# Performance work log

Measured on AMD Instinct MI355X. Metric: run time of the kernel, lower is better.

Reference implementation:

```python
import jax, jax.numpy as jnp
import numpy as np

N, E = 100000, 1600000
D_IN, D_HID, D_OUT, P_HID = 256, 128, 128, 512
BN_EPS = 1e-5


def setup_inputs():
    key = jax.random.key(0)
    ks = jax.random.split(key, 16)
    rn = lambda k, sh, s: jax.random.normal(k, sh, jnp.float32) * s
    inp = {
        "x1": rn(ks[0], (N, D_IN), 1.0),
        "x2": rn(ks[1], (N, D_IN), 1.0),
        "edge_index_v1": jax.random.randint(ks[2], (2, E), 0, N, dtype=jnp.int32),
        "edge_index_v2": jax.random.randint(ks[3], (2, E), 0, N, dtype=jnp.int32),
    }
    # student (s_) and teacher (t_) encoder params: GCN weight/bias, BN gamma/beta, PReLU a
    for i, p in enumerate(("s", "t")):
        kk = jax.random.split(ks[4 + i], 4)
        inp[p + "_W1"] = rn(kk[0], (D_IN, D_HID), (2.0 / (D_IN + D_HID)) ** 0.5)
        inp[p + "_b1"] = jnp.zeros((D_HID,), jnp.float32)
        inp[p + "_g1"] = jnp.ones((D_HID,), jnp.float32)
        inp[p + "_be1"] = jnp.zeros((D_HID,), jnp.float32)
        inp[p + "_a1"] = jnp.float32(0.25)
        inp[p + "_W2"] = rn(kk[1], (D_HID, D_OUT), (2.0 / (D_HID + D_OUT)) ** 0.5)
        inp[p + "_b2"] = jnp.zeros((D_OUT,), jnp.float32)
        inp[p + "_g2"] = jnp.ones((D_OUT,), jnp.float32)
        inp[p + "_be2"] = jnp.zeros((D_OUT,), jnp.float32)
        inp[p + "_a2"] = jnp.float32(0.25)
    kk = jax.random.split(ks[6], 2)
    inp["p_W1"] = rn(kk[0], (D_OUT, P_HID), (2.0 / (D_OUT + P_HID)) ** 0.5)
    inp["p_b1"] = jnp.full((P_HID,), 0.01, jnp.float32)
    inp["p_a"] = jnp.float32(0.25)
    inp["p_W2"] = rn(kk[1], (P_HID, D_OUT), (2.0 / (P_HID + D_OUT)) ** 0.5)
    inp["p_b2"] = jnp.full((D_OUT,), 0.01, jnp.float32)
    return inp


def _add_self_loops(edge_index, n):
    loops = jnp.arange(n, dtype=edge_index.dtype)
    return (jnp.concatenate([edge_index[0], loops]),
            jnp.concatenate([edge_index[1], loops]))


def _gcn(x, src, dst, W, b):
    # torch_geometric GCNConv: symmetric deg^-1/2 norm, transform then scatter-add, bias after
    n = x.shape[0]
    ew = jnp.ones(src.shape, x.dtype)
    deg = jax.ops.segment_sum(ew, dst, num_segments=n)
    dinv = jnp.where(deg > 0, jax.lax.rsqrt(deg), 0.0)
    norm = (dinv[src] * dinv[dst])[:, None]  # [E+N, 1]
    h = x @ W  # [N, d_out]
    out = jax.ops.segment_sum(h[src] * norm, dst, num_segments=n)
    return out + b


def _bn(x, g, b):
    mu = x.mean(0)
    var = ((x - mu) ** 2).mean(0)  # biased var, training-mode batch stats
    return (x - mu) * jax.lax.rsqrt(var + BN_EPS) * g + b


def _prelu(x, a):
    return jnp.where(x >= 0, x, a * x)


def _encoder(x, src, dst, p):
    W1, b1, g1, be1, a1, W2, b2, g2, be2, a2 = p
    h = _prelu(_bn(_gcn(x, src, dst, W1, b1), g1, be1), a1)
    return _prelu(_bn(_gcn(h, src, dst, W2, b2), g2, be2), a2)


def _normalize(x):
    return x / jnp.maximum(jnp.linalg.norm(x, axis=-1, keepdims=True), 1e-12)


def reference(x1, x2, edge_index_v1, edge_index_v2,
              s_W1, s_b1, s_g1, s_be1, s_a1, s_W2, s_b2, s_g2, s_be2, s_a2,
              t_W1, t_b1, t_g1, t_be1, t_a1, t_W2, t_b2, t_g2, t_be2, t_a2,
              p_W1, p_b1, p_a, p_W2, p_b2):
    n = x1.shape[0]
    src1, dst1 = _add_self_loops(edge_index_v1, n)
    src2, dst2 = _add_self_loops(edge_index_v2, n)
    sp = (s_W1, s_b1, s_g1, s_be1, s_a1, s_W2, s_b2, s_g2, s_be2, s_a2)
    tp = (t_W1, t_b1, t_g1, t_be1, t_a1, t_W2, t_b2, t_g2, t_be2, t_a2)

    v1_student = _encoder(x1, src1, dst1, sp)
    v2_student = _encoder(x2, src2, dst2, sp)

    def _pred(h):
        return _prelu(h @ p_W1 + p_b1, p_a) @ p_W2 + p_b2

    v1_pred = _pred(v1_student)
    v2_pred = _pred(v2_student)

    v1_teacher = jax.lax.stop_gradient(_encoder(x1, src1, dst1, tp))
    v2_teacher = jax.lax.stop_gradient(_encoder(x2, src2, dst2, tp))

    loss1 = 2.0 - 2.0 * (_normalize(v1_pred) * _normalize(v2_teacher)).sum(-1)
    loss2 = 2.0 - 2.0 * (_normalize(v2_pred) * _normalize(v1_teacher)).sum(-1)
    return (v1_student, v2_student, (loss1 + loss2).mean())
```

## Files before the change

kernel.cpp:

```cpp
#include <hip/hip_runtime.h>

#define NN 100000
#define EE 1600000
#define ENN (EE + NN)
#define DIN 256
#define DH 128
#define PH 512

static constexpr float BN_EPS_C = 1e-5f;

typedef __bf16 bf16_t;
typedef bf16_t bf16x8 __attribute__((ext_vector_type(8)));
typedef bf16_t bf16x4 __attribute__((ext_vector_type(4)));
typedef float floatx4 __attribute__((ext_vector_type(4)));


__global__ void init_deg_k(int* __restrict__ deg1, int* __restrict__ deg2) {
    int i = blockIdx.x * 256 + threadIdx.x;
    if (i < NN) { deg1[i] = 1; deg2[i] = 1; }
}

__global__ void count_deg_k(const int* __restrict__ dst, int* __restrict__ deg) {
    int e = blockIdx.x * 256 + threadIdx.x;
    if (e < EE) atomicAdd(&deg[dst[e]], 1);
}

__global__ void dinv_k(const int* __restrict__ deg, float* __restrict__ dinv) {
    int i = blockIdx.x * 256 + threadIdx.x;
    if (i < NN) dinv[i] = rsqrtf((float)deg[i]);
}

__global__ void scan1_k(const int* __restrict__ deg, int* __restrict__ bsum) {
    __shared__ int sh[256];
    int t = threadIdx.x;
    int base = blockIdx.x * 1024 + t * 4;
    int s = 0;
#pragma unroll
    for (int i = 0; i < 4; i++) { int idx = base + i; if (idx < NN) s += deg[idx]; }
    sh[t] = s; __syncthreads();
    for (int off = 128; off > 0; off >>= 1) { if (t < off) sh[t] += sh[t + off]; __syncthreads(); }
    if (t == 0) bsum[blockIdx.x] = sh[0];
}

__global__ void scan2_k(int* __restrict__ bsum, int nb) {
    __shared__ int sh[128];
    int t = threadIdx.x;
    int my = (t < nb) ? bsum[t] : 0;
    sh[t] = my; __syncthreads();
    for (int off = 1; off < 128; off <<= 1) {
        int v = (t >= off) ? sh[t - off] : 0;
        __syncthreads(); sh[t] += v; __syncthreads();
    }
    if (t < nb) bsum[t] = sh[t] - my;
}

__global__ void scan3_k(const int* __restrict__ deg, const int* __restrict__ bsum,
                        int* __restrict__ rowoff) {
    __shared__ int sh[256];
    int t = threadIdx.x;
    int base = blockIdx.x * 1024 + t * 4;
    int v[4]; int s = 0;
#pragma unroll
    for (int i = 0; i < 4; i++) { int idx = base + i; v[i] = (idx < NN) ? deg[idx] : 0; s += v[i]; }
    int my = s;
    sh[t] = s; __syncthreads();
    for (int off = 1; off < 256; off <<= 1) {
        int x = (t >= off) ? sh[t - off] : 0;
        __syncthreads(); sh[t] += x; __syncthreads();
    }
    int run = sh[t] - my + bsum[blockIdx.x];
#pragma unroll
    for (int i = 0; i < 4; i++) { int idx = base + i; if (idx < NN) rowoff[idx] = run; run += v[i]; }
    if (blockIdx.x == 0 && t == 0) rowoff[NN] = ENN;
}

__global__ void csr_init_k(const int* __restrict__ rowoff, const float* __restrict__ dinv,
                           int* __restrict__ cursor, int2* __restrict__ csre) {
    int i = blockIdx.x * 256 + threadIdx.x;
    if (i < NN) {
        int p = rowoff[i];
        float d = dinv[i];
        csre[p] = make_int2(i, __float_as_int(d * d));
        cursor[i] = p + 1;
    }
}

__global__ void csr_place_k(const int* __restrict__ src, const int* __restrict__ dst,
                            const float* __restrict__ dinv, int* __restrict__ cursor,
                            int2* __restrict__ csre) {
    int e = blockIdx.x * 256 + threadIdx.x;
    if (e < EE) {
        int s = src[e], d = dst[e];
        int p = atomicAdd(&cursor[d], 1);
        csre[p] = make_int2(s, __float_as_int(dinv[s] * dinv[d]));
    }
}


__global__ __launch_bounds__(256) void gather256_k(
    const int* __restrict__ ro, const int2* __restrict__ csre,
    const bf16_t* __restrict__ h,
    const float* __restrict__ bs, const float* __restrict__ bt,
    float* __restrict__ out)
{
    int wv = threadIdx.x >> 6, lane = threadIdx.x & 63;
    int d = blockIdx.x * 4 + wv;
    if (d >= NN) return;
    int beg = ro[d], end = ro[d + 1];
    int half = lane >> 5;
    int l32 = lane & 31;
    int c8 = l32 * 8;
    const bf16_t* hp = h + c8;
    float acc[8] = {0.f, 0.f, 0.f, 0.f, 0.f, 0.f, 0.f, 0.f};

    for (int e = beg; e < end; e += 8) {
        int i0 = e + half;
        int i1 = i0 + 2, i2 = i0 + 4, i3 = i0 + 6;
        bool val0 = i0 < end, val1 = i1 < end, val2 = i2 < end, val3 = i3 < end;
        int j0 = val0 ? i0 : end - 1;
        int j1 = val1 ? i1 : end - 1;
        int j2 = val2 ? i2 : end - 1;
        int j3 = val3 ? i3 : end - 1;
        int2 w0 = csre[j0];
        int2 w1 = csre[j1];
        int2 w2 = csre[j2];
        int2 w3 = csre[j3];
        uint4 p0 = *(const uint4*)(hp + w0.x * 256);
        uint4 p1 = *(const uint4*)(hp + w1.x * 256);
        uint4 p2 = *(const uint4*)(hp + w2.x * 256);
        uint4 p3 = *(const uint4*)(hp + w3.x * 256);
        float f0 = val0 ? __int_as_float(w0.y) : 0.f;
        float f1 = val1 ? __int_as_float(w1.y) : 0.f;
        float f2 = val2 ? __int_as_float(w2.y) : 0.f;
        float f3 = val3 ? __int_as_float(w3.y) : 0.f;
#define GACC(P, F) \
        acc[0] += (F) * __uint_as_float((P).x << 16); \
        acc[1] += (F) * __uint_as_float((P).x & 0xffff0000u); \
        acc[2] += (F) * __uint_as_float((P).y << 16); \
        acc[3] += (F) * __uint_as_float((P).y & 0xffff0000u); \
        acc[4] += (F) * __uint_as_float((P).z << 16); \
        acc[5] += (F) * __uint_as_float((P).z & 0xffff0000u); \
        acc[6] += (F) * __uint_as_float((P).w << 16); \
        acc[7] += (F) * __uint_as_float((P).w & 0xffff0000u);
        GACC(p0, f0)
        GACC(p1, f1)
        GACC(p2, f2)
        GACC(p3, f3)
#undef GACC
    }

#pragma unroll
    for (int j = 0; j < 8; j++) acc[j] += __shfl_xor(acc[j], 32);

    int cB = c8 + half * 4;
    int o = half * 4;
    float b0 = (cB < 128) ? bs[cB]     : bt[cB - 128];
    float b1 = (cB < 128) ? bs[cB + 1] : bt[cB - 127];
    float b2 = (cB < 128) ? bs[cB + 2] : bt[cB - 126];
    float b3 = (cB < 128) ? bs[cB + 3] : bt[cB - 125];
    float4 r = make_float4(acc[o] + b0, acc[o + 1] + b1, acc[o + 2] + b2, acc[o + 3] + b3);
    *(float4*)&out[(size_t)d * 256 + cB] = r;
}


#define GSTAT 1024
#define SROWS ((NN + GSTAT - 1) / GSTAT)

__global__ __launch_bounds__(256) void bn_stats_cat_k(const float* __restrict__ x,
                                                      float* __restrict__ stats) {
    __shared__ float sh[2][4][256];
    int t = threadIdx.x;
    int wv = t >> 6, lane = t & 63;
    int c4 = lane * 4;
    int rend = (blockIdx.x + 1) * SROWS; if (rend > NN) rend = NN;
    float4 s = make_float4(0.f, 0.f, 0.f, 0.f);
    float4 q = make_float4(0.f, 0.f, 0.f, 0.f);
    for (int r = blockIdx.x * SROWS + wv; r < rend; r += 4) {
        float4 v = *(const float4*)&x[(size_t)r * 256 + c4];
        s.x += v.x; s.y += v.y; s.z += v.z; s.w += v.w;
        q.x += v.x * v.x; q.y += v.y * v.y; q.z += v.z * v.z; q.w += v.w * v.w;
    }
    *(float4*)&sh[0][wv][c4] = s;
    *(float4*)&sh[1][wv][c4] = q;
    __syncthreads();
    if (t < 128) {
        int which = t >> 6;
        int c = (t & 63) * 4;
        float4 a  = *(float4*)&sh[which][0][c];
        float4 b  = *(float4*)&sh[which][1][c];
        float4 cc = *(float4*)&sh[which][2][c];
        float4 d  = *(float4*)&sh[which][3][c];
        atomicAdd(&stats[which * 256 + c],     a.x + b.x + cc.x + d.x);
        atomicAdd(&stats[which * 256 + c + 1], a.y + b.y + cc.y + d.y);
        atomicAdd(&stats[which * 256 + c + 2], a.z + b.z + cc.z + d.z);
        atomicAdd(&stats[which * 256 + c + 3], a.w + b.w + cc.w + d.w);
    }
}

__global__ void bn_prelu_cat_k(const float* __restrict__ x, const float* __restrict__ stats,
                               const float* __restrict__ gs, const float* __restrict__ gt,
                               const float* __restrict__ bes, const float* __restrict__ bet,
                               const float* __restrict__ as_, const float* __restrict__ at_,
                               bf16_t* __restrict__ out) {
    size_t i4 = ((size_t)blockIdx.x * 256 + threadIdx.x) * 4;
    if (i4 < (size_t)NN * 256) {
        int c = (int)(i4 & 255);
        bool st = c < 128;
        int cb = st ? c : c - 128;
        const float* gp  = st ? gs  : gt;
        const float* bep = st ? bes : bet;
        float al = st ? as_[0] : at_[0];
        float4 v = *(const float4*)&x[i4];
        float vv[4] = {v.x, v.y, v.z, v.w};
        bf16x4 o;
#pragma unroll
        for (int j = 0; j < 4; j++) {
            float mu  = stats[c + j] * (1.0f / NN);
            float var = stats[256 + c + j] * (1.0f / NN) - mu * mu;
            float sc  = rsqrtf(var + BN_EPS_C) * gp[cb + j];
            float r   = (vv[j] - mu) * sc + bep[cb + j];
            r = r >= 0.f ? r : al * r;
            o[j] = (bf16_t)r;
        }
        *(bf16x4*)&out[i4] = o;
    }
}

__global__ void bn_prelu_out_k(const float* __restrict__ x, const float* __restrict__ stats,
                               const float* __restrict__ gs, const float* __restrict__ gt,
                               const float* __restrict__ bes, const float* __restrict__ bet,
                               const float* __restrict__ as_, const float* __restrict__ at_,
                               float* __restrict__ outs, bf16_t* __restrict__ outsb,
                               bf16_t* __restrict__ outt) {
    size_t i4 = ((size_t)blockIdx.x * 256 + threadIdx.x) * 4;
    if (i4 >= (size_t)NN * 256) return;
    int c = (int)(i4 & 255);
    size_t r = i4 >> 8;
    bool st = c < 128;
    int cb = st ? c : c - 128;
    const float* gp  = st ? gs  : gt;
    const float* bep = st ? bes : bet;
    float al = st ? as_[0] : at_[0];
    float4 v = *(const float4*)&x[i4];
    float vv[4] = {v.x, v.y, v.z, v.w};
    float res[4];
    bf16x4 o;
#pragma unroll
    for (int j = 0; j < 4; j++) {
        float mu  = stats[c + j] * (1.0f / NN);
        float var = stats[256 + c + j] * (1.0f / NN) - mu * mu;
        float sc  = rsqrtf(var + BN_EPS_C) * gp[cb + j];
        float rr  = (vv[j] - mu) * sc + bep[cb + j];
        rr = rr >= 0.f ? rr : al * rr;
        res[j] = rr;
        o[j] = (bf16_t)rr;
    }
    if (st) {
        *(float4*)&outs[r * 128 + cb] = make_float4(res[0], res[1], res[2], res[3]);
        *(bf16x4*)&outsb[r * 128 + cb] = o;
    } else {
        *(bf16x4*)&outt[r * 128 + cb] = o;
    }
}


__global__ void wt_k(const float* __restrict__ W, bf16_t* __restrict__ Wt, int K, int M) {
    int i = blockIdx.x * 256 + threadIdx.x;
    if (i < K * M) {
        int k = i / M, m = i - k * M;
        Wt[(size_t)m * K + k] = (bf16_t)W[i];
    }
}


#define LDT 40

template <int K, typename AT, typename OT, bool BIAS, bool PRELU>
__global__ __launch_bounds__(256) void mgemm_k(
    const AT* __restrict__ A, int lda, const bf16_t* __restrict__ Wt,
    OT* __restrict__ C, int ldc, int nrows, int aoffy,
    const float* __restrict__ bias, const float* __restrict__ prelu_a)
{
    __shared__ __align__(16) bf16_t sA[128 * LDT];
    __shared__ __align__(16) bf16_t sB[128 * LDT];
    const int tid = threadIdx.x;
    const int row0 = blockIdx.x * 128;
    const int col0 = blockIdx.y * 128;
    const int lane = tid & 63, quad = lane >> 4, l15 = lane & 15;
    const int wv = tid >> 6, wrow = wv >> 1, wcol = wv & 1;

    const int sr = tid >> 1;
    const int sh = (tid & 1) * 16;

    floatx4 acc[4][4] = {};

    const int arow = row0 + sr;
    const bool arow_ok = arow < nrows;
    const AT*     ag = A  + (size_t)arow * lda + sh + blockIdx.y * aoffy;
    const bf16_t* bg = Wt + (size_t)(col0 + sr) * K + sh;

    for (int k0 = 0; k0 < K; k0 += 32) {
        __syncthreads();
        if constexpr (sizeof(AT) == 4) {
            float4 f0, f1, f2, f3;
            if (arow_ok) {
                const float4* p4 = (const float4*)(ag + k0);
                f0 = p4[0]; f1 = p4[1]; f2 = p4[2]; f3 = p4[3];
            } else {
                f0 = f1 = f2 = f3 = make_float4(0.f, 0.f, 0.f, 0.f);
            }
            bf16x8 u0 = {(bf16_t)f0.x, (bf16_t)f0.y, (bf16_t)f0.z, (bf16_t)f0.w,
                         (bf16_t)f1.x, (bf16_t)f1.y, (bf16_t)f1.z, (bf16_t)f1.w};
            bf16x8 u1 = {(bf16_t)f2.x, (bf16_t)f2.y, (bf16_t)f2.z, (bf16_t)f2.w,
                         (bf16_t)f3.x, (bf16_t)f3.y, (bf16_t)f3.z, (bf16_t)f3.w};
            *(bf16x8*)&sA[sr * LDT + sh]     = u0;
            *(bf16x8*)&sA[sr * LDT + sh + 8] = u1;
        } else {
            int4 w0, w1;
            if (arow_ok) {
                const int4* p4 = (const int4*)(ag + k0);
                w0 = p4[0]; w1 = p4[1];
            } else {
                w0 = make_int4(0, 0, 0, 0); w1 = make_int4(0, 0, 0, 0);
            }
            *(int4*)&sA[sr * LDT + sh]     = w0;
            *(int4*)&sA[sr * LDT + sh + 8] = w1;
        }
        {
            const int4* wp = (const int4*)(bg + k0);
            int4 w0 = wp[0], w1 = wp[1];
            *(int4*)&sB[sr * LDT + sh]     = w0;
            *(int4*)&sB[sr * LDT + sh + 8] = w1;
        }
        __syncthreads();

        bf16x8 af[4], bf[4];
#pragma unroll
        for (int r = 0; r < 4; r++)
            af[r] = *(const bf16x8*)&sA[(wrow * 64 + r * 16 + l15) * LDT + quad * 8];
#pragma unroll
        for (int c = 0; c < 4; c++)
            bf[c] = *(const bf16x8*)&sB[(wcol * 64 + c * 16 + l15) * LDT + quad * 8];
#pragma unroll
        for (int r = 0; r < 4; r++)
#pragma unroll
            for (int c = 0; c < 4; c++)
                acc[r][c] = __builtin_amdgcn_mfma_f32_16x16x32_bf16(af[r], bf[c], acc[r][c], 0, 0, 0);
    }

    const float alpha = PRELU ? prelu_a[0] : 0.f;
#pragma unroll
    for (int r = 0; r < 4; r++) {
        const int rbase = wrow * 64 + r * 16 + quad * 4;
#pragma unroll
        for (int c = 0; c < 4; c++) {
            const int gcol = col0 + wcol * 64 + c * 16 + l15;
            const float bv = BIAS ? bias[gcol] : 0.f;
#pragma unroll
            for (int j = 0; j < 4; j++) {
                const int grow = row0 + rbase + j;
                if (grow < nrows) {
                    float v = acc[r][c][j] + bv;
                    if (PRELU) v = v >= 0.f ? v : alpha * v;
                    C[(size_t)grow * ldc + gcol] = (OT)v;
                }
            }
        }
    }
}


__global__ void loss_partial_k(const bf16_t* __restrict__ v1p, const bf16_t* __restrict__ v2t,
                               const bf16_t* __restrict__ v2p, const bf16_t* __restrict__ v1t,
                               float* __restrict__ partials) {
    __shared__ float shw[4];
    int t = threadIdx.x;
    int lane = t & 63, wv = t >> 6;
    float wsum = 0.f;
    for (int it = 0; it < 8; ++it) {
        int r = blockIdx.x * 32 + wv * 8 + it;
        if (r < NN) {
            const bf16_t* A = v1p + (size_t)r * DH;
            const bf16_t* B = v2t + (size_t)r * DH;
            const bf16_t* Cc = v2p + (size_t)r * DH;
            const bf16_t* D = v1t + (size_t)r * DH;
            float a0 = (float)A[lane], a1 = (float)A[lane + 64];
            float b0 = (float)B[lane], b1 = (float)B[lane + 64];
            float c0 = (float)Cc[lane], c1 = (float)Cc[lane + 64];
            float d0 = (float)D[lane], d1 = (float)D[lane + 64];
            float dot1 = a0 * b0 + a1 * b1;
            float na = a0 * a0 + a1 * a1, nb = b0 * b0 + b1 * b1;
            float dot2 = c0 * d0 + c1 * d1;
            float nc = c0 * c0 + c1 * c1, nd = d0 * d0 + d1 * d1;
            for (int off = 32; off > 0; off >>= 1) {
                dot1 += __shfl_down(dot1, off);
                na   += __shfl_down(na, off);
                nb   += __shfl_down(nb, off);
                dot2 += __shfl_down(dot2, off);
                nc   += __shfl_down(nc, off);
                nd   += __shfl_down(nd, off);
            }
            if (lane == 0) {
                float den1 = fmaxf(sqrtf(na), 1e-12f) * fmaxf(sqrtf(nb), 1e-12f);
                float den2 = fmaxf(sqrtf(nc), 1e-12f) * fmaxf(sqrtf(nd), 1e-12f);
                wsum += 4.f - 2.f * dot1 / den1 - 2.f * dot2 / den2;
            }
        }
    }
    if (lane == 0) shw[wv] = wsum;
    __syncthreads();
    if (t == 0) partials[blockIdx.x] = shw[0] + shw[1] + shw[2] + shw[3];
}

__global__ void loss_final_k(const float* __restrict__ partials, int n, float* __restrict__ out) {
    __shared__ float sh[256];
    int t = threadIdx.x;
    float s = 0.f;
    for (int i = t; i < n; i += 256) s += partials[i];
    sh[t] = s; __syncthreads();
    for (int off = 128; off > 0; off >>= 1) { if (t < off) sh[t] += sh[t + off]; __syncthreads(); }
    if (t == 0) out[0] = sh[0] / (float)NN;
}


extern "C" void kernel_launch(void* const* d_in, const int* in_sizes, int n_in,
                              void* d_out, int out_size, void* d_ws, size_t ws_size,
                              hipStream_t stream) {
    const float* x1 = (const float*)d_in[0];
    const float* x2 = (const float*)d_in[1];
    const int* ei1 = (const int*)d_in[2];
    const int* ei2 = (const int*)d_in[3];
    const float* sp[10]; for (int i = 0; i < 10; i++) sp[i] = (const float*)d_in[4 + i];
    const float* tp[10]; for (int i = 0; i < 10; i++) tp[i] = (const float*)d_in[14 + i];
    const float* pW1 = (const float*)d_in[24];
    const float* pb1 = (const float*)d_in[25];
    const float* pa  = (const float*)d_in[26];
    const float* pW2 = (const float*)d_in[27];
    const float* pb2 = (const float*)d_in[28];

    float* out = (float*)d_out;
    float* v1s = out;
    float* v2s = out + (size_t)NN * DH;
    float* lossp = out + (size_t)2 * NN * DH;

    char* p = (char*)d_ws;
    auto alloc = [&](size_t bytes) { char* r = p; p += (bytes + 255) & ~(size_t)255; return r; };
    int*   deg1   = (int*)alloc(NN * 4);
    int*   deg2   = (int*)alloc(NN * 4);
    float* dinv1  = (float*)alloc(NN * 4);
    float* dinv2  = (float*)alloc(NN * 4);
    int*   ro1    = (int*)alloc((NN + 1) * 4);
    int*   ro2    = (int*)alloc((NN + 1) * 4);
    int*   cursor = (int*)alloc(NN * 4);
    int*   bsum   = (int*)alloc(128 * 4);
    int2*  csre1  = (int2*)alloc((size_t)ENN * 8);
    int2*  csre2  = (int2*)alloc((size_t)ENN * 8);
    bf16_t* hcat  = (bf16_t*)alloc((size_t)NN * 256 * 2);
    bf16_t* h2    = (bf16_t*)alloc((size_t)NN * 256 * 2);
    float*  agg   = (float*)alloc((size_t)NN * 256 * 4);
    bf16_t* v1sb  = (bf16_t*)alloc((size_t)NN * DH * 2);
    bf16_t* v2sb  = (bf16_t*)alloc((size_t)NN * DH * 2);
    bf16_t* v1t   = (bf16_t*)alloc((size_t)NN * DH * 2);
    bf16_t* v2t   = (bf16_t*)alloc((size_t)NN * DH * 2);
    bf16_t* v1p   = (bf16_t*)alloc((size_t)NN * DH * 2);
    bf16_t* v2p   = (bf16_t*)alloc((size_t)NN * DH * 2);
    float* stats  = (float*)alloc(4 * 512 * 4);
    float* partials = (float*)alloc(4096 * 4);
    bf16_t* W1cat = (bf16_t*)alloc((size_t)2 * DIN * DH * 2);
    bf16_t* W2cat = (bf16_t*)alloc((size_t)2 * DH * DH * 2);
    bf16_t* pW1t = (bf16_t*)alloc((size_t)DH * PH * 2);
    bf16_t* pW2t = (bf16_t*)alloc((size_t)PH * DH * 2);

    const int GN256 = (NN + 255) / 256;
    const int GE256 = (EE + 255) / 256;
    const int NB_SCAN = (NN + 1023) / 1024;
    const int GMM = (NN + 127) / 128;
    const int GG = (NN + 3) / 4;
    const int GEL4 = (NN * 256 / 4 + 255) / 256;

    hipMemsetAsync(stats, 0, 4 * 512 * 4, stream);

    wt_k<<<(DIN * DH + 255) / 256, 256, 0, stream>>>(sp[0], W1cat, DIN, DH);
    wt_k<<<(DIN * DH + 255) / 256, 256, 0, stream>>>(tp[0], W1cat + (size_t)DH * DIN, DIN, DH);
    wt_k<<<(DH * DH + 255) / 256, 256, 0, stream>>>(sp[5], W2cat, DH, DH);
    wt_k<<<(DH * DH + 255) / 256, 256, 0, stream>>>(tp[5], W2cat + (size_t)DH * DH, DH, DH);
    wt_k<<<(DH * PH + 255) / 256, 256, 0, stream>>>(pW1, pW1t, DH, PH);
    wt_k<<<(PH * DH + 255) / 256, 256, 0, stream>>>(pW2, pW2t, PH, DH);

    init_deg_k<<<GN256, 256, 0, stream>>>(deg1, deg2);
    count_deg_k<<<GE256, 256, 0, stream>>>(ei1 + EE, deg1);
    count_deg_k<<<GE256, 256, 0, stream>>>(ei2 + EE, deg2);
    dinv_k<<<GN256, 256, 0, stream>>>(deg1, dinv1);
    dinv_k<<<GN256, 256, 0, stream>>>(deg2, dinv2);

    scan1_k<<<NB_SCAN, 256, 0, stream>>>(deg1, bsum);
    scan2_k<<<1, 128, 0, stream>>>(bsum, NB_SCAN);
    scan3_k<<<NB_SCAN, 256, 0, stream>>>(deg1, bsum, ro1);
    csr_init_k<<<GN256, 256, 0, stream>>>(ro1, dinv1, cursor, csre1);
    csr_place_k<<<GE256, 256, 0, stream>>>(ei1, ei1 + EE, dinv1, cursor, csre1);

    scan1_k<<<NB_SCAN, 256, 0, stream>>>(deg2, bsum);
    scan2_k<<<1, 128, 0, stream>>>(bsum, NB_SCAN);
    scan3_k<<<NB_SCAN, 256, 0, stream>>>(deg2, bsum, ro2);
    csr_init_k<<<GN256, 256, 0, stream>>>(ro2, dinv2, cursor, csre2);
    csr_place_k<<<GE256, 256, 0, stream>>>(ei2, ei2 + EE, dinv2, cursor, csre2);

    auto encoder = [&](const float* x, const int* ro, const int2* csre,
                       float* vs_out, bf16_t* vsb, bf16_t* vt, int set) {
        mgemm_k<DIN, float, bf16_t, false, false><<<dim3(GMM, 2), 256, 0, stream>>>(
            x, DIN, W1cat, hcat, 256, NN, 0, nullptr, nullptr);
        gather256_k<<<GG, 256, 0, stream>>>(ro, csre, hcat, sp[1], tp[1], agg);
        bn_stats_cat_k<<<GSTAT, 256, 0, stream>>>(agg, stats + set * 512);
        bn_prelu_cat_k<<<GEL4, 256, 0, stream>>>(agg, stats + set * 512,
            sp[2], tp[2], sp[3], tp[3], sp[4], tp[4], hcat);
        mgemm_k<DH, bf16_t, bf16_t, false, false><<<dim3(GMM, 2), 256, 0, stream>>>(
            hcat, 256, W2cat, h2, 256, NN, 128, nullptr, nullptr);
        gather256_k<<<GG, 256, 0, stream>>>(ro, csre, h2, sp[6], tp[6], agg);
        bn_stats_cat_k<<<GSTAT, 256, 0, stream>>>(agg, stats + (set + 1) * 512);
        bn_prelu_out_k<<<GEL4, 256, 0, stream>>>(agg, stats + (set + 1) * 512,
            sp[7], tp[7], sp[8], tp[8], sp[9], tp[9], vs_out, vsb, vt);
    };

    encoder(x1, ro1, csre1, v1s, v1sb, v1t, 0);
    encoder(x2, ro2, csre2, v2s, v2sb, v2t, 2);

    bf16_t* hid = (bf16_t*)agg;
    auto predictor = [&](const bf16_t* vin, bf16_t* vout) {
        mgemm_k<DH, bf16_t, bf16_t, true, true><<<dim3(GMM, PH / 128), 256, 0, stream>>>(
            vin, DH, pW1t, hid, PH, NN, 0, pb1, pa);
        mgemm_k<PH, bf16_t, bf16_t, true, false><<<dim3(GMM, 1), 256, 0, stream>>>(
            hid, PH, pW2t, vout, DH, NN, 0, pb2, nullptr);
    };
    predictor(v1sb, v1p);
    predictor(v2sb, v2p);

    const int GL = (NN + 31) / 32;
    loss_partial_k<<<GL, 256, 0, stream>>>(v1p, v2t, v2p, v1t, partials);
    loss_final_k<<<1, 256, 0, stream>>>(partials, GL, lossp);
}
```

Measured before the change: 2.041 ms.

## Fuse BN statistics into gather, BN-PReLU into GEMM load, batch predictor views

```diff
diff --git a/kernel.cpp b/kernel.cpp
--- a/kernel.cpp
+++ b/kernel.cpp
@@ -97,92 +97,82 @@
 }
 
 
+#define GGB 2048
+
 __global__ __launch_bounds__(256) void gather256_k(
     const int* __restrict__ ro, const int2* __restrict__ csre,
     const bf16_t* __restrict__ h,
     const float* __restrict__ bs, const float* __restrict__ bt,
-    float* __restrict__ out)
+    float* __restrict__ out, float* __restrict__ stats)
 {
     int wv = threadIdx.x >> 6, lane = threadIdx.x & 63;
-    int d = blockIdx.x * 4 + wv;
-    if (d >= NN) return;
-    int beg = ro[d], end = ro[d + 1];
     int half = lane >> 5;
     int l32 = lane & 31;
     int c8 = l32 * 8;
     const bf16_t* hp = h + c8;
-    float acc[8] = {0.f, 0.f, 0.f, 0.f, 0.f, 0.f, 0.f, 0.f};
-
-    for (int e = beg; e < end; e += 8) {
-        int i0 = e + half;
-        int i1 = i0 + 2, i2 = i0 + 4, i3 = i0 + 6;
-        bool val0 = i0 < end, val1 = i1 < end, val2 = i2 < end, val3 = i3 < end;
-        int j0 = val0 ? i0 : end - 1;
-        int j1 = val1 ? i1 : end - 1;
-        int j2 = val2 ? i2 : end - 1;
-        int j3 = val3 ? i3 : end - 1;
-        int2 w0 = csre[j0];
-        int2 w1 = csre[j1];
-        int2 w2 = csre[j2];
-        int2 w3 = csre[j3];
-        uint4 p0 = *(const uint4*)(hp + w0.x * 256);
-        uint4 p1 = *(const uint4*)(hp + w1.x * 256);
-        uint4 p2 = *(const uint4*)(hp + w2.x * 256);
-        uint4 p3 = *(const uint4*)(hp + w3.x * 256);
-        float f0 = val0 ? __int_as_float(w0.y) : 0.f;
-        float f1 = val1 ? __int_as_float(w1.y) : 0.f;
-        float f2 = val2 ? __int_as_float(w2.y) : 0.f;
-        float f3 = val3 ? __int_as_float(w3.y) : 0.f;
-#define GACC(P, F) \
-        acc[0] += (F) * __uint_as_float((P).x << 16); \
-        acc[1] += (F) * __uint_as_float((P).x & 0xffff0000u); \
-        acc[2] += (F) * __uint_as_float((P).y << 16); \
-        acc[3] += (F) * __uint_as_float((P).y & 0xffff0000u); \
-        acc[4] += (F) * __uint_as_float((P).z << 16); \
-        acc[5] += (F) * __uint_as_float((P).z & 0xffff0000u); \
-        acc[6] += (F) * __uint_as_float((P).w << 16); \
-        acc[7] += (F) * __uint_as_float((P).w & 0xffff0000u);
-        GACC(p0, f0)
-        GACC(p1, f1)
-        GACC(p2, f2)
-        GACC(p3, f3)
-#undef GACC
-    }
-
-#pragma unroll
-    for (int j = 0; j < 8; j++) acc[j] += __shfl_xor(acc[j], 32);
-
     int cB = c8 + half * 4;
-    int o = half * 4;
     float b0 = (cB < 128) ? bs[cB]     : bt[cB - 128];
     float b1 = (cB < 128) ? bs[cB + 1] : bt[cB - 127];
     float b2 = (cB < 128) ? bs[cB + 2] : bt[cB - 126];
     float b3 = (cB < 128) ? bs[cB + 3] : bt[cB - 125];
-    float4 r = make_float4(acc[o] + b0, acc[o + 1] + b1, acc[o + 2] + b2, acc[o + 3] + b3);
-    *(float4*)&out[(size_t)d * 256 + cB] = r;
-}
-
-
-#define GSTAT 1024
-#define SROWS ((NN + GSTAT - 1) / GSTAT)
-
-__global__ __launch_bounds__(256) void bn_stats_cat_k(const float* __restrict__ x,
-                                                      float* __restrict__ stats) {
+    float s0 = 0.f, s1 = 0.f, s2 = 0.f, s3 = 0.f;
+    float q0 = 0.f, q1 = 0.f, q2 = 0.f, q3 = 0.f;
+
+    for (int d = blockIdx.x * 4 + wv; d < NN; d += GGB * 4) {
+        int beg = ro[d], end = ro[d + 1];
+        float acc[8] = {0.f, 0.f, 0.f, 0.f, 0.f, 0.f, 0.f, 0.f};
+        for (int e = beg; e < end; e += 8) {
+            int i0 = e + half;
+            int i1 = i0 + 2, i2 = i0 + 4, i3 = i0 + 6;
+            bool val0 = i0 < end, val1 = i1 < end, val2 = i2 < end, val3 = i3 < end;
+            int j0 = val0 ? i0 : end - 1;
+            int j1 = val1 ? i1 : end - 1;
+            int j2 = val2 ? i2 : end - 1;
+            int j3 = val3 ? i3 : end - 1;
+            int2 w0 = csre[j0];
+            int2 w1 = csre[j1];
+            int2 w2 = csre[j2];
+            int2 w3 = csre[j3];
+            uint4 p0 = *(const uint4*)(hp + w0.x * 256);
+            uint4 p1 = *(const uint4*)(hp + w1.x * 256);
+            uint4 p2 = *(const uint4*)(hp + w2.x * 256);
+            uint4 p3 = *(const uint4*)(hp + w3.x * 256);
+            float f0 = val0 ? __int_as_float(w0.y) : 0.f;
+            float f1 = val1 ? __int_as_float(w1.y) : 0.f;
+            float f2 = val2 ? __int_as_float(w2.y) : 0.f;
+            float f3 = val3 ? __int_as_float(w3.y) : 0.f;
+#define GACC(P, F) \
+            acc[0] += (F) * __uint_as_float((P).x << 16); \
+            acc[1] += (F) * __uint_as_float((P).x & 0xffff0000u); \
+            acc[2] += (F) * __uint_as_float((P).y << 16); \
+            acc[3] += (F) * __uint_as_float((P).y & 0xffff0000u); \
+            acc[4] += (F) * __uint_as_float((P).z << 16); \
+            acc[5] += (F) * __uint_as_float((P).z & 0xffff0000u); \
+            acc[6] += (F) * __uint_as_float((P).w << 16); \
+            acc[7] += (F) * __uint_as_float((P).w & 0xffff0000u);
+            GACC(p0, f0)
+            GACC(p1, f1)
+            GACC(p2, f2)
+            GACC(p3, f3)
+#undef GACC
+        }
+
+#pragma unroll
+        for (int j = 0; j < 8; j++) acc[j] += __shfl_xor(acc[j], 32);
+
+        int o = half * 4;
+        float r0 = acc[o] + b0, r1 = acc[o + 1] + b1;
+        float r2 = acc[o + 2] + b2, r3 = acc[o + 3] + b3;
+        *(float4*)&out[(size_t)d * 256 + cB] = make_float4(r0, r1, r2, r3);
+        s0 += r0; s1 += r1; s2 += r2; s3 += r3;
+        q0 += r0 * r0; q1 += r1 * r1; q2 += r2 * r2; q3 += r3 * r3;
+    }
+
     __shared__ float sh[2][4][256];
+    *(float4*)&sh[0][wv][cB] = make_float4(s0, s1, s2, s3);
+    *(float4*)&sh[1][wv][cB] = make_float4(q0, q1, q2, q3);
+    __syncthreads();
     int t = threadIdx.x;
-    int wv = t >> 6, lane = t & 63;
-    int c4 = lane * 4;
-    int rend = (blockIdx.x + 1) * SROWS; if (rend > NN) rend = NN;
-    float4 s = make_float4(0.f, 0.f, 0.f, 0.f);
-    float4 q = make_float4(0.f, 0.f, 0.f, 0.f);
-    for (int r = blockIdx.x * SROWS + wv; r < rend; r += 4) {
-        float4 v = *(const float4*)&x[(size_t)r * 256 + c4];
-        s.x += v.x; s.y += v.y; s.z += v.z; s.w += v.w;
-        q.x += v.x * v.x; q.y += v.y * v.y; q.z += v.z * v.z; q.w += v.w * v.w;
-    }
-    *(float4*)&sh[0][wv][c4] = s;
-    *(float4*)&sh[1][wv][c4] = q;
-    __syncthreads();
     if (t < 128) {
         int which = t >> 6;
         int c = (t & 63) * 4;
@@ -197,33 +187,19 @@
     }
 }
 
-__global__ void bn_prelu_cat_k(const float* __restrict__ x, const float* __restrict__ stats,
-                               const float* __restrict__ gs, const float* __restrict__ gt,
-                               const float* __restrict__ bes, const float* __restrict__ bet,
-                               const float* __restrict__ as_, const float* __restrict__ at_,
-                               bf16_t* __restrict__ out) {
-    size_t i4 = ((size_t)blockIdx.x * 256 + threadIdx.x) * 4;
-    if (i4 < (size_t)NN * 256) {
-        int c = (int)(i4 & 255);
-        bool st = c < 128;
-        int cb = st ? c : c - 128;
-        const float* gp  = st ? gs  : gt;
-        const float* bep = st ? bes : bet;
-        float al = st ? as_[0] : at_[0];
-        float4 v = *(const float4*)&x[i4];
-        float vv[4] = {v.x, v.y, v.z, v.w};
-        bf16x4 o;
-#pragma unroll
-        for (int j = 0; j < 4; j++) {
-            float mu  = stats[c + j] * (1.0f / NN);
-            float var = stats[256 + c + j] * (1.0f / NN) - mu * mu;
-            float sc  = rsqrtf(var + BN_EPS_C) * gp[cb + j];
-            float r   = (vv[j] - mu) * sc + bep[cb + j];
-            r = r >= 0.f ? r : al * r;
-            o[j] = (bf16_t)r;
-        }
-        *(bf16x4*)&out[i4] = o;
-    }
+
+__global__ void bn_coef_k(const float* __restrict__ stats,
+                          const float* __restrict__ gs, const float* __restrict__ gt,
+                          const float* __restrict__ bes, const float* __restrict__ bet,
+                          float* __restrict__ co) {
+    int c = threadIdx.x;
+    float mu  = stats[c] * (1.0f / NN);
+    float var = stats[256 + c] * (1.0f / NN) - mu * mu;
+    float g  = (c < 128) ? gs[c]  : gt[c - 128];
+    float be = (c < 128) ? bes[c] : bet[c - 128];
+    float sc = rsqrtf(var + BN_EPS_C) * g;
+    co[c] = sc;
+    co[256 + c] = be - mu * sc;
 }
 
 __global__ void bn_prelu_out_k(const float* __restrict__ x, const float* __restrict__ stats,
@@ -275,11 +251,13 @@
 
 #define LDT 40
 
-template <int K, typename AT, typename OT, bool BIAS, bool PRELU>
+template <int K, typename AT, typename OT, bool BIAS, bool PRELU, bool BNF>
 __global__ __launch_bounds__(256) void mgemm_k(
     const AT* __restrict__ A, int lda, const bf16_t* __restrict__ Wt,
     OT* __restrict__ C, int ldc, int nrows, int aoffy,
-    const float* __restrict__ bias, const float* __restrict__ prelu_a)
+    const float* __restrict__ bias, const float* __restrict__ prelu_a,
+    const float* __restrict__ bnco, const float* __restrict__ bnal_s,
+    const float* __restrict__ bnal_t)
 {
     __shared__ __align__(16) bf16_t sA[128 * LDT];
     __shared__ __align__(16) bf16_t sB[128 * LDT];
@@ -298,6 +276,9 @@
     const bool arow_ok = arow < nrows;
     const AT*     ag = A  + (size_t)arow * lda + sh + blockIdx.y * aoffy;
     const bf16_t* bg = Wt + (size_t)(col0 + sr) * K + sh;
+
+    float bnal = 0.f;
+    if constexpr (BNF) bnal = (blockIdx.y == 0) ? bnal_s[0] : bnal_t[0];
 
     for (int k0 = 0; k0 < K; k0 += 32) {
         __syncthreads();
@@ -308,6 +289,23 @@
                 f0 = p4[0]; f1 = p4[1]; f2 = p4[2]; f3 = p4[3];
             } else {
                 f0 = f1 = f2 = f3 = make_float4(0.f, 0.f, 0.f, 0.f);
+            }
+            if constexpr (BNF) {
+                const int cbch = (int)blockIdx.y * 128 + k0 + sh;
+                const float4* sc4 = (const float4*)&bnco[cbch];
+                const float4* sh4 = (const float4*)&bnco[256 + cbch];
+                float4 scv[4] = {sc4[0], sc4[1], sc4[2], sc4[3]};
+                float4 shv[4] = {sh4[0], sh4[1], sh4[2], sh4[3]};
+                float4* fp[4] = {&f0, &f1, &f2, &f3};
+#pragma unroll
+                for (int u = 0; u < 4; u++) {
+                    float4 f = *fp[u];
+                    f.x = f.x * scv[u].x + shv[u].x; f.x = f.x >= 0.f ? f.x : bnal * f.x;
+                    f.y = f.y * scv[u].y + shv[u].y; f.y = f.y >= 0.f ? f.y : bnal * f.y;
+                    f.z = f.z * scv[u].z + shv[u].z; f.z = f.z >= 0.f ? f.z : bnal * f.z;
+                    f.w = f.w * scv[u].w + shv[u].w; f.w = f.w >= 0.f ? f.w : bnal * f.w;
+                    *fp[u] = f;
+                }
             }
             bf16x8 u0 = {(bf16_t)f0.x, (bf16_t)f0.y, (bf16_t)f0.z, (bf16_t)f0.w,
                          (bf16_t)f1.x, (bf16_t)f1.y, (bf16_t)f1.z, (bf16_t)f1.w};
@@ -465,6 +463,7 @@
     bf16_t* v1p   = (bf16_t*)alloc((size_t)NN * DH * 2);
     bf16_t* v2p   = (bf16_t*)alloc((size_t)NN * DH * 2);
     float* stats  = (float*)alloc(4 * 512 * 4);
+    float* bnco   = (float*)alloc(512 * 4);
     float* partials = (float*)alloc(4096 * 4);
     bf16_t* W1cat = (bf16_t*)alloc((size_t)2 * DIN * DH * 2);
     bf16_t* W2cat = (bf16_t*)alloc((size_t)2 * DH * DH * 2);
@@ -475,7 +474,7 @@
     const int GE256 = (EE + 255) / 256;
     const int NB_SCAN = (NN + 1023) / 1024;
     const int GMM = (NN + 127) / 128;
-    const int GG = (NN + 3) / 4;
+    const int GMM2 = (2 * NN + 127) / 128;
     const int GEL4 = (NN * 256 / 4 + 255) / 256;
 
     hipMemsetAsync(stats, 0, 4 * 512 * 4, stream);
@@ -507,16 +506,15 @@
 
     auto encoder = [&](const float* x, const int* ro, const int2* csre,
                        float* vs_out, bf16_t* vsb, bf16_t* vt, int set) {
-        mgemm_k<DIN, float, bf16_t, false, false><<<dim3(GMM, 2), 256, 0, stream>>>(
-            x, DIN, W1cat, hcat, 256, NN, 0, nullptr, nullptr);
-        gather256_k<<<GG, 256, 0, stream>>>(ro, csre, hcat, sp[1], tp[1], agg);
-        bn_stats_cat_k<<<GSTAT, 256, 0, stream>>>(agg, stats + set * 512);
-        bn_prelu_cat_k<<<GEL4, 256, 0, stream>>>(agg, stats + set * 512,
-            sp[2], tp[2], sp[3], tp[3], sp[4], tp[4], hcat);
-        mgemm_k<DH, bf16_t, bf16_t, false, false><<<dim3(GMM, 2), 256, 0, stream>>>(
-            hcat, 256, W2cat, h2, 256, NN, 128, nullptr, nullptr);
-        gather256_k<<<GG, 256, 0, stream>>>(ro, csre, h2, sp[6], tp[6], agg);
-        bn_stats_cat_k<<<GSTAT, 256, 0, stream>>>(agg, stats + (set + 1) * 512);
+        mgemm_k<DIN, float, bf16_t, false, false, false><<<dim3(GMM, 2), 256, 0, stream>>>(
+            x, DIN, W1cat, hcat, 256, NN, 0, nullptr, nullptr, nullptr, nullptr, nullptr);
+        gather256_k<<<GGB, 256, 0, stream>>>(ro, csre, hcat, sp[1], tp[1], agg,
+                                             stats + set * 512);
+        bn_coef_k<<<1, 256, 0, stream>>>(stats + set * 512, sp[2], tp[2], sp[3], tp[3], bnco);
+        mgemm_k<DH, float, bf16_t, false, false, true><<<dim3(GMM, 2), 256, 0, stream>>>(
+            agg, 256, W2cat, h2, 256, NN, 128, nullptr, nullptr, bnco, sp[4], tp[4]);
+        gather256_k<<<GGB, 256, 0, stream>>>(ro, csre, h2, sp[6], tp[6], agg,
+                                             stats + (set + 1) * 512);
         bn_prelu_out_k<<<GEL4, 256, 0, stream>>>(agg, stats + (set + 1) * 512,
             sp[7], tp[7], sp[8], tp[8], sp[9], tp[9], vs_out, vsb, vt);
     };
@@ -524,15 +522,11 @@
     encoder(x1, ro1, csre1, v1s, v1sb, v1t, 0);
     encoder(x2, ro2, csre2, v2s, v2sb, v2t, 2);
 
-    bf16_t* hid = (bf16_t*)agg;
-    auto predictor = [&](const bf16_t* vin, bf16_t* vout) {
-        mgemm_k<DH, bf16_t, bf16_t, true, true><<<dim3(GMM, PH / 128), 256, 0, stream>>>(
-            vin, DH, pW1t, hid, PH, NN, 0, pb1, pa);
-        mgemm_k<PH, bf16_t, bf16_t, true, false><<<dim3(GMM, 1), 256, 0, stream>>>(
-            hid, PH, pW2t, vout, DH, NN, 0, pb2, nullptr);
-    };
-    predictor(v1sb, v1p);
-    predictor(v2sb, v2p);
+    bf16_t* hid2 = (bf16_t*)hcat;
+    mgemm_k<DH, bf16_t, bf16_t, true, true, false><<<dim3(GMM2, PH / 128), 256, 0, stream>>>(
+        v1sb, DH, pW1t, hid2, PH, 2 * NN, 0, pb1, pa, nullptr, nullptr, nullptr);
+    mgemm_k<PH, bf16_t, bf16_t, true, false, false><<<dim3(GMM2, 1), 256, 0, stream>>>(
+        hid2, PH, pW2t, v1p, DH, 2 * NN, 0, pb2, nullptr, nullptr, nullptr, nullptr);
 
     const int GL = (NN + 31) / 32;
     loss_partial_k<<<GL, 256, 0, stream>>>(v1p, v2t, v2p, v1t, partials);
```

Result: slower. 2.192 ms (+7.4%).
